# Performance work log

Measured on AMD Instinct MI355X. Metric: run time of the kernel, lower is better.

Reference implementation:

```python
import jax, jax.numpy as jnp
import numpy as np

B, S, D = 2, 2048, 2048
H, KV, HD = 8, 1, 256          # num_heads, num_kv_heads, head_dim
ROPE_BASE = 10000.0
NEG_INF = -1e9


def _rope_cos_sin(position_ids, head_dim, base):
    # position_ids: [B, S] -> cos/sin: [B, S, head_dim]
    inv_freq = 1.0 / (base ** (jnp.arange(0, head_dim, 2, dtype=jnp.float32) / head_dim))
    freqs = position_ids.astype(jnp.float32)[..., None] * inv_freq  # [B,S,HD/2]
    emb = jnp.concatenate([freqs, freqs], axis=-1)                  # [B,S,HD]
    return jnp.cos(emb), jnp.sin(emb)


def _rotate_half(x):
    h = x.shape[-1] // 2
    return jnp.concatenate([-x[..., h:], x[..., :h]], axis=-1)


def _apply_rope(x, cos, sin):
    # x: [B,h,S,HD]; cos/sin: [B,S,HD]
    c = cos[:, None, :, :]
    s = sin[:, None, :, :]
    return x * c + _rotate_half(x) * s


def setup_inputs() -> dict:
    key = jax.random.key(0)
    ks = jax.random.split(key, 6)
    hidden_state = jax.random.normal(ks[0], (B, S, D), dtype=jnp.float32)
    # additive causal mask: 0 on/below diagonal, -inf above
    causal = jnp.tril(jnp.ones((S, S), dtype=bool))
    attention_mask = jnp.where(causal, 0.0, NEG_INF).astype(jnp.float32)[None, None]  # [B?1,1,S,S]
    attention_mask = jnp.broadcast_to(attention_mask, (B, 1, S, S))
    position_ids = jnp.broadcast_to(jnp.arange(S, dtype=jnp.int64)[None, :], (B, S))
    scale = 0.02
    Wq = jax.random.normal(ks[1], (D, H * HD), dtype=jnp.float32) * scale
    Wk = jax.random.normal(ks[2], (D, KV * HD), dtype=jnp.float32) * scale
    Wv = jax.random.normal(ks[3], (D, KV * HD), dtype=jnp.float32) * scale
    Wo = jax.random.normal(ks[4], (H * HD, D), dtype=jnp.float32) * scale
    return {"hidden_state": hidden_state, "attention_mask": attention_mask,
            "position_ids": position_ids, "Wq": Wq, "Wk": Wk, "Wv": Wv, "Wo": Wo}


def reference(hidden_state, attention_mask, position_ids, Wq, Wk, Wv, Wo):
    bsz, q_len, _ = hidden_state.shape
    n_rep = H // KV
    # projections
    q = (hidden_state @ Wq).reshape(bsz, q_len, H, HD).transpose(0, 2, 1, 3)   # [B,H,S,HD]
    k = (hidden_state @ Wk).reshape(bsz, q_len, KV, HD).transpose(0, 2, 1, 3)  # [B,KV,S,HD]
    v = (hidden_state @ Wv).reshape(bsz, q_len, KV, HD).transpose(0, 2, 1, 3)
    # RoPE
    cos, sin = _rope_cos_sin(position_ids, HD, ROPE_BASE)
    q = _apply_rope(q, cos, sin)
    k = _apply_rope(k, cos, sin)
    # GQA: repeat kv heads
    k = jnp.repeat(k, n_rep, axis=1)  # [B,H,S,HD]
    v = jnp.repeat(v, n_rep, axis=1)
    # eager attention with full score matrix (faithful to source)
    scores = jnp.einsum('bhqd,bhkd->bhqk', q, k) / jnp.sqrt(jnp.float32(HD))
    scores = scores + attention_mask
    attn = jax.nn.softmax(scores.astype(jnp.float32), axis=-1).astype(q.dtype)
    out = jnp.einsum('bhqk,bhkd->bhqd', attn, v)            # [B,H,S,HD]
    out = out.transpose(0, 2, 1, 3).reshape(bsz, q_len, H * HD)
    return out @ Wo
```

## Files before the change

kernel.cpp:

```cpp
#include <hip/hip_runtime.h>
#include <cstdint>
#include <cstddef>

#define B_   2
#define S_   2048
#define D_   2048
#define H_   8
#define HD_  256
#define M_   (B_ * S_)
#define NQ_  (H_ * HD_)
#define NKV_ 256

typedef unsigned short u16;
typedef __attribute__((ext_vector_type(8))) short short8v;
typedef __attribute__((ext_vector_type(4))) float f32x4;

__device__ __forceinline__ u16 f2bf_rn(float x) {
    unsigned int u = __float_as_uint(x);
    unsigned int r = u + 0x7FFFu + ((u >> 16) & 1u);
    return (u16)(r >> 16);
}
__device__ __forceinline__ float bf2f(u16 h) {
    return __uint_as_float(((unsigned int)h) << 16);
}

__device__ __forceinline__ void gll16(const u16* g, u16* l) {
    __builtin_amdgcn_global_load_lds(
        (const __attribute__((address_space(1))) void*)(g),
        (__attribute__((address_space(3))) void*)(l), 16, 0, 0);
}

__global__ __launch_bounds__(256) void split_kernel(const float* __restrict__ in,
                                                    u16* __restrict__ hi,
                                                    u16* __restrict__ lo)
{
    const size_t i = ((size_t)blockIdx.x * 256 + threadIdx.x) * 8;
    float4 v0 = *(const float4*)(in + i);
    float4 v1 = *(const float4*)(in + i + 4);
    float xs[8] = {v0.x, v0.y, v0.z, v0.w, v1.x, v1.y, v1.z, v1.w};
    unsigned int hv[4], lv[4];
#pragma unroll
    for (int k = 0; k < 4; ++k) {
        u16 h0 = f2bf_rn(xs[2 * k]);
        u16 h1 = f2bf_rn(xs[2 * k + 1]);
        u16 l0 = f2bf_rn(xs[2 * k] - bf2f(h0));
        u16 l1 = f2bf_rn(xs[2 * k + 1] - bf2f(h1));
        hv[k] = (unsigned int)h0 | ((unsigned int)h1 << 16);
        lv[k] = (unsigned int)l0 | ((unsigned int)l1 << 16);
    }
    *(uint4*)(hi + i) = make_uint4(hv[0], hv[1], hv[2], hv[3]);
    *(uint4*)(lo + i) = make_uint4(lv[0], lv[1], lv[2], lv[3]);
}

__global__ __launch_bounds__(256) void tsplit_kernel(const float* __restrict__ W,
                                                     u16* __restrict__ Th,
                                                     u16* __restrict__ Tl,
                                                     int K, int N)
{
    __shared__ float t[64][65];
    const int kt = blockIdx.x, nt = blockIdx.y;
    const int c4 = (threadIdx.x & 15) * 4;
    const int r  = threadIdx.x >> 4;

#pragma unroll
    for (int s = 0; s < 4; ++s) {
        const int kk = r + s * 16;
        float4 v = *(const float4*)(W + (size_t)(kt * 64 + kk) * N + nt * 64 + c4);
        t[kk][c4 + 0] = v.x;
        t[kk][c4 + 1] = v.y;
        t[kk][c4 + 2] = v.z;
        t[kk][c4 + 3] = v.w;
    }
    __syncthreads();
#pragma unroll
    for (int s = 0; s < 4; ++s) {
        const int nn = r + s * 16;
        unsigned int hv[2], lv[2];
#pragma unroll
        for (int p = 0; p < 2; ++p) {
            u16 h0, h1, l0, l1;
            float x0 = t[c4 + 2 * p][nn];
            float x1 = t[c4 + 2 * p + 1][nn];
            h0 = f2bf_rn(x0); l0 = f2bf_rn(x0 - bf2f(h0));
            h1 = f2bf_rn(x1); l1 = f2bf_rn(x1 - bf2f(h1));
            hv[p] = (unsigned int)h0 | ((unsigned int)h1 << 16);
            lv[p] = (unsigned int)l0 | ((unsigned int)l1 << 16);
        }
        u16* ph = Th + (size_t)(nt * 64 + nn) * K + kt * 64 + c4;
        u16* pl = Tl + (size_t)(nt * 64 + nn) * K + kt * 64 + c4;
        *(uint2*)ph = make_uint2(hv[0], hv[1]);
        *(uint2*)pl = make_uint2(lv[0], lv[1]);
    }
}

__device__ __forceinline__ void mfma_gemm_tile(
    const u16* __restrict__ Ah, const u16* __restrict__ Al,
    const u16* __restrict__ Bh, const u16* __restrict__ Bl,
    float* __restrict__ C, const int Kd, const int ldc,
    const int bm0, const int bn0)
{
    __shared__ u16 ldsAh[128 * 32];
    __shared__ u16 ldsAl[128 * 32];
    __shared__ u16 ldsBh[128 * 32];
    __shared__ u16 ldsBl[128 * 32];

    const int tid  = threadIdx.x;
    const int lane = tid & 63;
    const int w    = tid >> 6;
    const int wr   = w >> 1, wc = w & 1;

    const int srow = w * 32 + (lane >> 2);
    const int schk = (lane & 3) * 8;
    const u16* gAh = Ah + (size_t)(bm0 + srow) * Kd + schk;
    const u16* gAl = Al + (size_t)(bm0 + srow) * Kd + schk;
    const u16* gBh = Bh + (size_t)(bn0 + srow) * Kd + schk;
    const u16* gBl = Bl + (size_t)(bn0 + srow) * Kd + schk;

    f32x4 acc[4][4];
#pragma unroll
    for (int i = 0; i < 4; ++i)
#pragma unroll
        for (int j = 0; j < 4; ++j) acc[i][j] = (f32x4){0.f, 0.f, 0.f, 0.f};

    const int fr = lane & 15;
    const int kb = (lane >> 4) * 8;

    for (int k0 = 0; k0 < Kd; k0 += 32) {
        if (k0) __syncthreads();
#pragma unroll
        for (int c = 0; c < 2; ++c) {
            const size_t go = (size_t)(c * 16) * Kd + k0;
            const int lb = (w * 32 + c * 16) * 32;
            gll16(gAh + go, &ldsAh[lb]);
            gll16(gAl + go, &ldsAl[lb]);
            gll16(gBh + go, &ldsBh[lb]);
            gll16(gBl + go, &ldsBl[lb]);
        }
        __syncthreads();

        short8v a_h[4], a_l[4], b_h[4], b_l[4];
#pragma unroll
        for (int f = 0; f < 4; ++f) {
            const int ra = (wr * 64 + f * 16 + fr) * 32 + kb;
            const int rb = (wc * 64 + f * 16 + fr) * 32 + kb;
            a_h[f] = *(const short8v*)&ldsAh[ra];
            a_l[f] = *(const short8v*)&ldsAl[ra];
            b_h[f] = *(const short8v*)&ldsBh[rb];
            b_l[f] = *(const short8v*)&ldsBl[rb];
        }
#pragma unroll
        for (int i = 0; i < 4; ++i)
#pragma unroll
            for (int j = 0; j < 4; ++j) {
                acc[i][j] = __builtin_amdgcn_mfma_f32_16x16x32_bf16(a_h[i], b_h[j], acc[i][j], 0, 0, 0);
                acc[i][j] = __builtin_amdgcn_mfma_f32_16x16x32_bf16(a_h[i], b_l[j], acc[i][j], 0, 0, 0);
                acc[i][j] = __builtin_amdgcn_mfma_f32_16x16x32_bf16(a_l[i], b_h[j], acc[i][j], 0, 0, 0);
            }
    }

    const int cr = (lane >> 4) * 4;
    const int cc = lane & 15;
#pragma unroll
    for (int i = 0; i < 4; ++i)
#pragma unroll
        for (int j = 0; j < 4; ++j) {
#pragma unroll
            for (int r = 0; r < 4; ++r) {
                C[(size_t)(bm0 + wr * 64 + i * 16 + cr + r) * ldc
                  + (bn0 + wc * 64 + j * 16 + cc)] = acc[i][j][r];
            }
        }
}

__global__ __launch_bounds__(256, 2) void qkv_mfma_kernel(
    const u16* __restrict__ Xh, const u16* __restrict__ Xl,
    const u16* __restrict__ WqTh, const u16* __restrict__ WqTl,
    const u16* __restrict__ WkTh, const u16* __restrict__ WkTl,
    const u16* __restrict__ WvTh, const u16* __restrict__ WvTl,
    float* __restrict__ Qo, float* __restrict__ Ko, float* __restrict__ Vo)
{
    const int bn = blockIdx.x;
    const u16 *Bh, *Bl; float* C; int ldc, col0;
    if (bn < 16)      { Bh = WqTh; Bl = WqTl; C = Qo; ldc = NQ_;  col0 = bn * 128; }
    else if (bn < 18) { Bh = WkTh; Bl = WkTl; C = Ko; ldc = NKV_; col0 = (bn - 16) * 128; }
    else              { Bh = WvTh; Bl = WvTl; C = Vo; ldc = NKV_; col0 = (bn - 18) * 128; }
    mfma_gemm_tile(Xh, Xl, Bh, Bl, C, D_, ldc, blockIdx.y * 128, col0);
}

__global__ __launch_bounds__(256, 2) void out_mfma_kernel(
    const u16* __restrict__ Ch, const u16* __restrict__ Cl,
    const u16* __restrict__ WoTh, const u16* __restrict__ WoTl,
    float* __restrict__ Out)
{
    mfma_gemm_tile(Ch, Cl, WoTh, WoTl, Out, NQ_, D_, blockIdx.y * 128, blockIdx.x * 128);
}

__global__ __launch_bounds__(128) void rope_split_q_kernel(
    const float* __restrict__ Qw, u16* __restrict__ Qh, u16* __restrict__ Ql)
{
    const int row = blockIdx.x;
    const int d = threadIdx.x;
    const int s = row & (S_ - 1);

    const float expo = (float)(2 * d) / (float)HD_;
    const float inv_freq = 1.0f / powf(10000.0f, expo);
    float sn, c;
    sincosf((float)s * inv_freq, &sn, &c);

    const float* qr = Qw + (size_t)row * NQ_;
    u16* qhr = Qh + (size_t)row * NQ_;
    u16* qlr = Ql + (size_t)row * NQ_;
#pragma unroll
    for (int h = 0; h < H_; ++h) {
        float x0 = qr[h * HD_ + d];
        float x1 = qr[h * HD_ + d + 128];
        float y0 = x0 * c - x1 * sn;
        float y1 = x1 * c + x0 * sn;
        u16 h0 = f2bf_rn(y0), h1 = f2bf_rn(y1);
        qhr[h * HD_ + d]       = h0;
        qhr[h * HD_ + d + 128] = h1;
        qlr[h * HD_ + d]       = f2bf_rn(y0 - bf2f(h0));
        qlr[h * HD_ + d + 128] = f2bf_rn(y1 - bf2f(h1));
    }
}

__global__ __launch_bounds__(128) void rope_split_k_swz_kernel(
    const float* __restrict__ Kw, u16* __restrict__ Kh, u16* __restrict__ Kl,
    int* __restrict__ wq)
{
    if (blockIdx.x == 0 && threadIdx.x == 0) *wq = 0;

    const int row = blockIdx.x;
    const int d = threadIdx.x;
    const int s = row & (S_ - 1);
    const int xm = row & 7;

    const float expo = (float)(2 * d) / (float)HD_;
    const float inv_freq = 1.0f / powf(10000.0f, expo);
    float sn, c;
    sincosf((float)s * inv_freq, &sn, &c);

    const float* kr = Kw + (size_t)row * HD_;
    float x0 = kr[d], x1 = kr[d + 128];
    float y0 = x0 * c - x1 * sn;
    float y1 = x1 * c + x0 * sn;
    u16 h0 = f2bf_rn(y0), h1 = f2bf_rn(y1);

    const int o0 = (((d >> 3) ^ xm) << 3) | (d & 7);
    const int o1 = ((((d + 128) >> 3) ^ xm) << 3) | (d & 7);
    Kh[(size_t)row * HD_ + o0] = h0;
    Kh[(size_t)row * HD_ + o1] = h1;
    Kl[(size_t)row * HD_ + o0] = f2bf_rn(y0 - bf2f(h0));
    Kl[(size_t)row * HD_ + o1] = f2bf_rn(y1 - bf2f(h1));
}

#define KVB_ 32
#define PBS_ 44
#define NITEM_ 512

__global__ __launch_bounds__(256, 2) void attn_mfma_kernel(
    const u16* __restrict__ Qh, const u16* __restrict__ Ql,
    const u16* __restrict__ Kh, const u16* __restrict__ Kl,
    const u16* __restrict__ VtH, const u16* __restrict__ VtL,
    u16* __restrict__ Ch, u16* __restrict__ Cl,
    int* __restrict__ wq)
{
    __shared__ u16 kvK[2 * 32 * 256];
    __shared__ u16 kvV[2 * 256 * 32];
    __shared__ u16 pb[2 * 64 * PBS_];
    __shared__ int s_item;

    const int tid = threadIdx.x;
    const int lane = tid & 63;
    const int w = tid >> 6;

    const int fr = lane & 15;
    const int kq = (lane >> 4);
    const int xm = fr & 7;

    const int k_hi = (lane >> 5);
    const int k_ch = lane & 31;
    const int v_dl = w * 64 + (lane >> 2);
    const int v_cc = (lane & 3) * 8;

    while (true) {
        __syncthreads();
        if (tid == 0) s_item = atomicAdd(wq, 1);
        __syncthreads();
        const int item = s_item;
        if (item >= NITEM_) break;

        const int qt = (item < 256) ? (31 - (item >> 4)) : ((item - 256) >> 4);
        const int bh = item & 15;
        const int b = bh >> 3, h = bh & 7;

        short8v qfh[8], qfl[8];
        {
            const size_t qrow = (size_t)(b * S_ + qt * 64 + w * 16 + fr);
            const u16* ph = Qh + qrow * NQ_ + h * HD_ + kq * 8;
            const u16* pl = Ql + qrow * NQ_ + h * HD_ + kq * 8;
#pragma unroll
            for (int ks = 0; ks < 8; ++ks) {
                qfh[ks] = *(const short8v*)(ph + ks * 32);
                qfl[ks] = *(const short8v*)(pl + ks * 32);
            }
        }

        f32x4 oacc[16];
#pragma unroll
        for (int f = 0; f < 16; ++f) oacc[f] = (f32x4){0.f, 0.f, 0.f, 0.f};
        float m_i[4] = {-1e30f, -1e30f, -1e30f, -1e30f};
        float l_i[4] = {0.f, 0.f, 0.f, 0.f};

        const u16* ksrc[2] = {Kh + (size_t)b * S_ * HD_, Kl + (size_t)b * S_ * HD_};
        const u16* vsrc[2] = {VtH + (size_t)b * HD_ * S_, VtL + (size_t)b * HD_ * S_};

        const int nkt = (qt + 1) * 2;

#define STAGE_K(KT)                                                            \
        {                                                                      \
            _Pragma("unroll")                                                  \
            for (int c = 0; c < 2; ++c) {                                      \
                _Pragma("unroll")                                              \
                for (int t = 0; t < 4; ++t) {                                  \
                    const int rl = w * 8 + t * 2 + k_hi;                       \
                    gll16(ksrc[c] + (size_t)((KT) * KVB_ + rl) * HD_ + k_ch * 8, \
                          &kvK[c * 8192 + (w * 2048 + t * 512)]);              \
                }                                                              \
            }                                                                  \
        }

#define STAGE_V(KT)                                                            \
        {                                                                      \
            _Pragma("unroll")                                                  \
            for (int c = 0; c < 2; ++c) {                                      \
                _Pragma("unroll")                                              \
                for (int t = 0; t < 4; ++t) {                                  \
                    gll16(vsrc[c] + (size_t)(v_dl + t * 16) * S_ + (KT) * KVB_ + v_cc, \
                          &kvV[c * 8192 + (w * 2048 + t * 512)]);              \
                }                                                              \
            }                                                                  \
        }

        STAGE_K(0)
        STAGE_V(0)
        __syncthreads();

        for (int kt = 0; kt < nkt; ++kt) {
            const bool more = (kt + 1 < nkt);

            f32x4 s0 = (f32x4){0.f, 0.f, 0.f, 0.f};
            f32x4 s1 = (f32x4){0.f, 0.f, 0.f, 0.f};
#pragma unroll
            for (int ks = 0; ks < 8; ++ks) {
                const int ch = (ks * 4 + kq) ^ xm;
                short8v kh0 = *(const short8v*)&kvK[fr * 256 + ch * 8];
                short8v kh1 = *(const short8v*)&kvK[(16 + fr) * 256 + ch * 8];
                short8v kl0 = *(const short8v*)&kvK[8192 + fr * 256 + ch * 8];
                short8v kl1 = *(const short8v*)&kvK[8192 + (16 + fr) * 256 + ch * 8];
                s0 = __builtin_amdgcn_mfma_f32_16x16x32_bf16(qfh[ks], kh0, s0, 0, 0, 0);
                s1 = __builtin_amdgcn_mfma_f32_16x16x32_bf16(qfh[ks], kh1, s1, 0, 0, 0);
                s0 = __builtin_amdgcn_mfma_f32_16x16x32_bf16(qfh[ks], kl0, s0, 0, 0, 0);
                s1 = __builtin_amdgcn_mfma_f32_16x16x32_bf16(qfh[ks], kl1, s1, 0, 0, 0);
                s0 = __builtin_amdgcn_mfma_f32_16x16x32_bf16(qfl[ks], kh0, s0, 0, 0, 0);
                s1 = __builtin_amdgcn_mfma_f32_16x16x32_bf16(qfl[ks], kh1, s1, 0, 0, 0);
            }

            const int qglob = qt * 64 + w * 16 + kq * 4;
            const int kg = kt * KVB_ + fr;
            float x0v[4], x1v[4], mxl[4];
            bool needl = false;
#pragma unroll
            for (int r = 0; r < 4; ++r) {
                float x0 = s0[r] * 0.0625f;
                float x1 = s1[r] * 0.0625f;
                if (kg > qglob + r)      x0 = -1e30f;
                if (kg + 16 > qglob + r) x1 = -1e30f;
                x0v[r] = x0; x1v[r] = x1;
                mxl[r] = fmaxf(x0, x1);
                needl = needl || (mxl[r] > m_i[r] + 8.0f);
            }
            if (__any((int)needl)) {
#pragma unroll
                for (int r = 0; r < 4; ++r) {
                    float mx = mxl[r];
#pragma unroll
                    for (int off = 1; off < 16; off <<= 1)
                        mx = fmaxf(mx, __shfl_xor(mx, off, 64));
                    const float mnew = fmaxf(m_i[r], mx);
                    const float alpha = __expf(m_i[r] - mnew);
                    l_i[r] *= alpha;
                    m_i[r] = mnew;
#pragma unroll
                    for (int f = 0; f < 16; ++f) oacc[f][r] *= alpha;
                }
            }
#pragma unroll
            for (int r = 0; r < 4; ++r) {
                const float p0 = __expf(x0v[r] - m_i[r]);
                const float p1 = __expf(x1v[r] - m_i[r]);
                float ps = p0 + p1;
#pragma unroll
                for (int off = 1; off < 16; off <<= 1)
                    ps += __shfl_xor(ps, off, 64);
                l_i[r] += ps;

                const int prow = (w * 16 + kq * 4 + r) * PBS_;
                u16 h0 = f2bf_rn(p0), h1 = f2bf_rn(p1);
                pb[prow + fr]                    = h0;
                pb[prow + 16 + fr]               = h1;
                pb[64 * PBS_ + prow + fr]        = f2bf_rn(p0 - bf2f(h0));
                pb[64 * PBS_ + prow + 16 + fr]   = f2bf_rn(p1 - bf2f(h1));
            }
            __syncthreads();

            if (more) STAGE_K(kt + 1)

            {
                short8v pah = *(const short8v*)&pb[(w * 16 + fr) * PBS_ + kq * 8];
                short8v pal = *(const short8v*)&pb[64 * PBS_ + (w * 16 + fr) * PBS_ + kq * 8];
#pragma unroll
                for (int f = 0; f < 16; ++f) {
                    const int vrow = (f * 16 + fr) * 32 + kq * 8;
                    short8v vh = *(const short8v*)&kvV[vrow];
                    short8v vl = *(const short8v*)&kvV[8192 + vrow];
                    oacc[f] = __builtin_amdgcn_mfma_f32_16x16x32_bf16(pah, vh, oacc[f], 0, 0, 0);
                    oacc[f] = __builtin_amdgcn_mfma_f32_16x16x32_bf16(pal, vh, oacc[f], 0, 0, 0);
                    oacc[f] = __builtin_amdgcn_mfma_f32_16x16x32_bf16(pah, vl, oacc[f], 0, 0, 0);
                }
            }
            if (more) {
                __syncthreads();
                STAGE_V(kt + 1)
            }
        }

        {
            const size_t obase = (size_t)(b * S_ + qt * 64 + w * 16 + kq * 4) * NQ_ + h * HD_ + fr;
            u16* ohr = Ch + obase;
            u16* olr = Cl + obase;
#pragma unroll
            for (int r = 0; r < 4; ++r) {
                const float inv_l = 1.0f / l_i[r];
#pragma unroll
                for (int f = 0; f < 16; ++f) {
                    const float v = oacc[f][r] * inv_l;
                    const u16 hh = f2bf_rn(v);
                    ohr[(size_t)r * NQ_ + f * 16] = hh;
                    olr[(size_t)r * NQ_ + f * 16] = f2bf_rn(v - bf2f(hh));
                }
            }
        }
#undef STAGE_K
#undef STAGE_V
    }
}

extern "C" void kernel_launch(void* const* d_in, const int* in_sizes, int n_in,
                              void* d_out, int out_size, void* d_ws, size_t ws_size,
                              hipStream_t stream)
{
    (void)in_sizes; (void)n_in; (void)out_size; (void)ws_size;

    const float* hidden = (const float*)d_in[0];
    const float* Wq = (const float*)d_in[3];
    const float* Wk = (const float*)d_in[4];
    const float* Wv = (const float*)d_in[5];
    const float* Wo = (const float*)d_in[6];
    float* out = (float*)d_out;

    char* ws = (char*)d_ws;
    float* Qw = (float*)(ws + 0);
    u16* Kh2 = (u16*)(ws + 0);
    u16* Kl2 = (u16*)(ws + 2097152u);
    u16* VtH = (u16*)(ws + 4194304u);
    u16* VtL = (u16*)(ws + 6291456u);
    int* wq  = (int*)(ws + 8388608u);
    float* Kw = (float*)(ws + 33554432u);
    float* Vw = (float*)(ws + 37748736u);
    u16* Ch2 = (u16*)(ws + 41943040u);
    u16* Cl2 = (u16*)(ws + 58720256u);
    u16* Ah  = (u16*)(ws + 75497472u);
    u16* Al  = (u16*)(ws + 92274688u);
    u16* WqTh = (u16*)(ws + 109051904u);
    u16* WqTl = (u16*)(ws + 117440512u);
    u16* WkTh = (u16*)(ws + 125829120u);
    u16* WkTl = (u16*)(ws + 126877696u);
    u16* WvTh = (u16*)(ws + 127926272u);
    u16* WvTl = (u16*)(ws + 128974848u);
    u16* WoTh = WqTh;
    u16* WoTl = WqTl;
    u16* Qhb = Ah;
    u16* Qlb = Al;

    split_kernel<<<dim3((M_ * D_) / (256 * 8)), dim3(256), 0, stream>>>(hidden, Ah, Al);

    tsplit_kernel<<<dim3(D_ / 64, NQ_ / 64),  dim3(256), 0, stream>>>(Wq, WqTh, WqTl, D_, NQ_);
    tsplit_kernel<<<dim3(D_ / 64, NKV_ / 64), dim3(256), 0, stream>>>(Wk, WkTh, WkTl, D_, NKV_);
    tsplit_kernel<<<dim3(D_ / 64, NKV_ / 64), dim3(256), 0, stream>>>(Wv, WvTh, WvTl, D_, NKV_);

    qkv_mfma_kernel<<<dim3(20, M_ / 128), dim3(256), 0, stream>>>(
        Ah, Al, WqTh, WqTl, WkTh, WkTl, WvTh, WvTl, Qw, Kw, Vw);

    rope_split_q_kernel<<<dim3(M_), dim3(128), 0, stream>>>(Qw, Qhb, Qlb);
    rope_split_k_swz_kernel<<<dim3(M_), dim3(128), 0, stream>>>(Kw, Kh2, Kl2, wq);

    tsplit_kernel<<<dim3(S_ / 64, NKV_ / 64), dim3(256), 0, stream>>>(
        Vw, VtH, VtL, S_, NKV_);
    tsplit_kernel<<<dim3(S_ / 64, NKV_ / 64), dim3(256), 0, stream>>>(
        Vw + (size_t)S_ * NKV_, VtH + (size_t)HD_ * S_, VtL + (size_t)HD_ * S_, S_, NKV_);

    attn_mfma_kernel<<<dim3(512), dim3(256), 0, stream>>>(
        Qhb, Qlb, Kh2, Kl2, VtH, VtL, Ch2, Cl2, wq);

    tsplit_kernel<<<dim3(NQ_ / 64, D_ / 64), dim3(256), 0, stream>>>(Wo, WoTh, WoTl, NQ_, D_);

    out_mfma_kernel<<<dim3(D_ / 128, M_ / 128), dim3(256), 0, stream>>>(
        Ch2, Cl2, WoTh, WoTl, out);
}
```

Before: 585.5 us.

## Make attention waves independent with direct global K/V loads and static scheduling

The attention kernel no longer stages K and V tiles through shared memory with block-wide barriers and an atomic work queue. Each wave now owns its own 16-row query slice, assigned statically from the block index, and reads K and V fragments straight from global memory, relying on L2/L1 caching. K is stored unswizzled to match. This removes barriers, the atomic queue and LDS staging, but makes each wave re-read K/V from cache rather than sharing tiles across the four waves. It also replaces dynamic load balancing with a fixed long-first ordering. The causal split is finer at 16 rows per wave.

```diff
diff --git a/kernel.cpp b/kernel.cpp
--- a/kernel.cpp
+++ b/kernel.cpp
@@ -224,16 +224,12 @@
     }
 }
 
-__global__ __launch_bounds__(128) void rope_split_k_swz_kernel(
-    const float* __restrict__ Kw, u16* __restrict__ Kh, u16* __restrict__ Kl,
-    int* __restrict__ wq)
-{
-    if (blockIdx.x == 0 && threadIdx.x == 0) *wq = 0;
-
+__global__ __launch_bounds__(128) void rope_split_k_kernel(
+    const float* __restrict__ Kw, u16* __restrict__ Kh, u16* __restrict__ Kl)
+{
     const int row = blockIdx.x;
     const int d = threadIdx.x;
     const int s = row & (S_ - 1);
-    const int xm = row & 7;
 
     const float expo = (float)(2 * d) / (float)HD_;
     const float inv_freq = 1.0f / powf(10000.0f, expo);
@@ -245,30 +241,21 @@
     float y0 = x0 * c - x1 * sn;
     float y1 = x1 * c + x0 * sn;
     u16 h0 = f2bf_rn(y0), h1 = f2bf_rn(y1);
-
-    const int o0 = (((d >> 3) ^ xm) << 3) | (d & 7);
-    const int o1 = ((((d + 128) >> 3) ^ xm) << 3) | (d & 7);
-    Kh[(size_t)row * HD_ + o0] = h0;
-    Kh[(size_t)row * HD_ + o1] = h1;
-    Kl[(size_t)row * HD_ + o0] = f2bf_rn(y0 - bf2f(h0));
-    Kl[(size_t)row * HD_ + o1] = f2bf_rn(y1 - bf2f(h1));
-}
-
-#define KVB_ 32
+    Kh[(size_t)row * HD_ + d]       = h0;
+    Kh[(size_t)row * HD_ + d + 128] = h1;
+    Kl[(size_t)row * HD_ + d]       = f2bf_rn(y0 - bf2f(h0));
+    Kl[(size_t)row * HD_ + d + 128] = f2bf_rn(y1 - bf2f(h1));
+}
+
 #define PBS_ 44
-#define NITEM_ 512
 
 __global__ __launch_bounds__(256, 2) void attn_mfma_kernel(
     const u16* __restrict__ Qh, const u16* __restrict__ Ql,
     const u16* __restrict__ Kh, const u16* __restrict__ Kl,
     const u16* __restrict__ VtH, const u16* __restrict__ VtL,
-    u16* __restrict__ Ch, u16* __restrict__ Cl,
-    int* __restrict__ wq)
-{
-    __shared__ u16 kvK[2 * 32 * 256];
-    __shared__ u16 kvV[2 * 256 * 32];
+    u16* __restrict__ Ch, u16* __restrict__ Cl)
+{
     __shared__ u16 pb[2 * 64 * PBS_];
-    __shared__ int s_item;
 
     const int tid = threadIdx.x;
     const int lane = tid & 63;
@@ -276,183 +263,135 @@
 
     const int fr = lane & 15;
     const int kq = (lane >> 4);
-    const int xm = fr & 7;
-
-    const int k_hi = (lane >> 5);
-    const int k_ch = lane & 31;
-    const int v_dl = w * 64 + (lane >> 2);
-    const int v_cc = (lane & 3) * 8;
-
-    while (true) {
-        __syncthreads();
-        if (tid == 0) s_item = atomicAdd(wq, 1);
-        __syncthreads();
-        const int item = s_item;
-        if (item >= NITEM_) break;
-
-        const int qt = (item < 256) ? (31 - (item >> 4)) : ((item - 256) >> 4);
-        const int bh = item & 15;
-        const int b = bh >> 3, h = bh & 7;
-
-        short8v qfh[8], qfl[8];
+
+    const int g = blockIdx.x * 4 + w;
+    const int j = g >> 4;
+    const int bh = g & 15;
+    const int qg = (j < 64) ? (127 - j) : (j - 64);
+    const int b = bh >> 3, h = bh & 7;
+
+    short8v qfh[8], qfl[8];
+    {
+        const size_t qrow = (size_t)(b * S_ + qg * 16 + fr);
+        const u16* ph = Qh + qrow * NQ_ + h * HD_ + kq * 8;
+        const u16* pl = Ql + qrow * NQ_ + h * HD_ + kq * 8;
+#pragma unroll
+        for (int ks = 0; ks < 8; ++ks) {
+            qfh[ks] = *(const short8v*)(ph + ks * 32);
+            qfl[ks] = *(const short8v*)(pl + ks * 32);
+        }
+    }
+
+    f32x4 oacc[16];
+#pragma unroll
+    for (int f = 0; f < 16; ++f) oacc[f] = (f32x4){0.f, 0.f, 0.f, 0.f};
+    float m_i[4] = {-1e30f, -1e30f, -1e30f, -1e30f};
+    float l_i[4] = {0.f, 0.f, 0.f, 0.f};
+
+    const u16* kbh = Kh + (size_t)(b * S_ + fr) * HD_ + kq * 8;
+    const u16* kbl = Kl + (size_t)(b * S_ + fr) * HD_ + kq * 8;
+    const u16* vbh = VtH + (size_t)(b * HD_ + fr) * S_ + kq * 8;
+    const u16* vbl = VtL + (size_t)(b * HD_ + fr) * S_ + kq * 8;
+
+    const int nkt = (qg >> 1) + 1;
+
+    for (int kt = 0; kt < nkt; ++kt) {
+        f32x4 s0 = (f32x4){0.f, 0.f, 0.f, 0.f};
+        f32x4 s1 = (f32x4){0.f, 0.f, 0.f, 0.f};
+        const u16* kh_p = kbh + (size_t)(kt * 32) * HD_;
+        const u16* kl_p = kbl + (size_t)(kt * 32) * HD_;
+#pragma unroll
+        for (int ks = 0; ks < 8; ++ks) {
+            short8v kh0 = *(const short8v*)(kh_p + ks * 32);
+            short8v kh1 = *(const short8v*)(kh_p + 16 * HD_ + ks * 32);
+            short8v kl0 = *(const short8v*)(kl_p + ks * 32);
+            short8v kl1 = *(const short8v*)(kl_p + 16 * HD_ + ks * 32);
+            s0 = __builtin_amdgcn_mfma_f32_16x16x32_bf16(qfh[ks], kh0, s0, 0, 0, 0);
+            s1 = __builtin_amdgcn_mfma_f32_16x16x32_bf16(qfh[ks], kh1, s1, 0, 0, 0);
+            s0 = __builtin_amdgcn_mfma_f32_16x16x32_bf16(qfh[ks], kl0, s0, 0, 0, 0);
+            s1 = __builtin_amdgcn_mfma_f32_16x16x32_bf16(qfh[ks], kl1, s1, 0, 0, 0);
+            s0 = __builtin_amdgcn_mfma_f32_16x16x32_bf16(qfl[ks], kh0, s0, 0, 0, 0);
+            s1 = __builtin_amdgcn_mfma_f32_16x16x32_bf16(qfl[ks], kh1, s1, 0, 0, 0);
+        }
+
+        const int qglob = qg * 16 + kq * 4;
+        const int kg = kt * 32 + fr;
+        float x0v[4], x1v[4], mxl[4];
+        bool needl = false;
+#pragma unroll
+        for (int r = 0; r < 4; ++r) {
+            float x0 = s0[r] * 0.0625f;
+            float x1 = s1[r] * 0.0625f;
+            if (kg > qglob + r)      x0 = -1e30f;
+            if (kg + 16 > qglob + r) x1 = -1e30f;
+            x0v[r] = x0; x1v[r] = x1;
+            mxl[r] = fmaxf(x0, x1);
+            needl = needl || (mxl[r] > m_i[r] + 8.0f);
+        }
+        if (__any((int)needl)) {
+#pragma unroll
+            for (int r = 0; r < 4; ++r) {
+                float mx = mxl[r];
+#pragma unroll
+                for (int off = 1; off < 16; off <<= 1)
+                    mx = fmaxf(mx, __shfl_xor(mx, off, 64));
+                const float mnew = fmaxf(m_i[r], mx);
+                const float alpha = __expf(m_i[r] - mnew);
+                l_i[r] *= alpha;
+                m_i[r] = mnew;
+#pragma unroll
+                for (int f = 0; f < 16; ++f) oacc[f][r] *= alpha;
+            }
+        }
+#pragma unroll
+        for (int r = 0; r < 4; ++r) {
+            const float p0 = __expf(x0v[r] - m_i[r]);
+            const float p1 = __expf(x1v[r] - m_i[r]);
+            float ps = p0 + p1;
+#pragma unroll
+            for (int off = 1; off < 16; off <<= 1)
+                ps += __shfl_xor(ps, off, 64);
+            l_i[r] += ps;
+
+            const int prow = (w * 16 + kq * 4 + r) * PBS_;
+            u16 h0 = f2bf_rn(p0), h1 = f2bf_rn(p1);
+            pb[prow + fr]                    = h0;
+            pb[prow + 16 + fr]               = h1;
+            pb[64 * PBS_ + prow + fr]        = f2bf_rn(p0 - bf2f(h0));
+            pb[64 * PBS_ + prow + 16 + fr]   = f2bf_rn(p1 - bf2f(h1));
+        }
+
         {
-            const size_t qrow = (size_t)(b * S_ + qt * 64 + w * 16 + fr);
-            const u16* ph = Qh + qrow * NQ_ + h * HD_ + kq * 8;
-            const u16* pl = Ql + qrow * NQ_ + h * HD_ + kq * 8;
-#pragma unroll
-            for (int ks = 0; ks < 8; ++ks) {
-                qfh[ks] = *(const short8v*)(ph + ks * 32);
-                qfl[ks] = *(const short8v*)(pl + ks * 32);
+            short8v pah = *(const short8v*)&pb[(w * 16 + fr) * PBS_ + kq * 8];
+            short8v pal = *(const short8v*)&pb[64 * PBS_ + (w * 16 + fr) * PBS_ + kq * 8];
+            const u16* vh_p = vbh + kt * 32;
+            const u16* vl_p = vbl + kt * 32;
+#pragma unroll
+            for (int f = 0; f < 16; ++f) {
+                short8v vh = *(const short8v*)(vh_p + (size_t)(f * 16) * S_);
+                short8v vl = *(const short8v*)(vl_p + (size_t)(f * 16) * S_);
+                oacc[f] = __builtin_amdgcn_mfma_f32_16x16x32_bf16(pah, vh, oacc[f], 0, 0, 0);
+                oacc[f] = __builtin_amdgcn_mfma_f32_16x16x32_bf16(pal, vh, oacc[f], 0, 0, 0);
+                oacc[f] = __builtin_amdgcn_mfma_f32_16x16x32_bf16(pah, vl, oacc[f], 0, 0, 0);
             }
         }
-
-        f32x4 oacc[16];
-#pragma unroll
-        for (int f = 0; f < 16; ++f) oacc[f] = (f32x4){0.f, 0.f, 0.f, 0.f};
-        float m_i[4] = {-1e30f, -1e30f, -1e30f, -1e30f};
-        float l_i[4] = {0.f, 0.f, 0.f, 0.f};
-
-        const u16* ksrc[2] = {Kh + (size_t)b * S_ * HD_, Kl + (size_t)b * S_ * HD_};
-        const u16* vsrc[2] = {VtH + (size_t)b * HD_ * S_, VtL + (size_t)b * HD_ * S_};
-
-        const int nkt = (qt + 1) * 2;
-
-#define STAGE_K(KT)                                                            \
-        {                                                                      \
-            _Pragma("unroll")                                                  \
-            for (int c = 0; c < 2; ++c) {                                      \
-                _Pragma("unroll")                                              \
-                for (int t = 0; t < 4; ++t) {                                  \
-                    const int rl = w * 8 + t * 2 + k_hi;                       \
-                    gll16(ksrc[c] + (size_t)((KT) * KVB_ + rl) * HD_ + k_ch * 8, \
-                          &kvK[c * 8192 + (w * 2048 + t * 512)]);              \
-                }                                                              \
-            }                                                                  \
-        }
-
-#define STAGE_V(KT)                                                            \
-        {                                                                      \
-            _Pragma("unroll")                                                  \
-            for (int c = 0; c < 2; ++c) {                                      \
-                _Pragma("unroll")                                              \
-                for (int t = 0; t < 4; ++t) {                                  \
-                    gll16(vsrc[c] + (size_t)(v_dl + t * 16) * S_ + (KT) * KVB_ + v_cc, \
-                          &kvV[c * 8192 + (w * 2048 + t * 512)]);              \
-                }                                                              \
-            }                                                                  \
-        }
-
-        STAGE_K(0)
-        STAGE_V(0)
-        __syncthreads();
-
-        for (int kt = 0; kt < nkt; ++kt) {
-            const bool more = (kt + 1 < nkt);
-
-            f32x4 s0 = (f32x4){0.f, 0.f, 0.f, 0.f};
-            f32x4 s1 = (f32x4){0.f, 0.f, 0.f, 0.f};
-#pragma unroll
-            for (int ks = 0; ks < 8; ++ks) {
-                const int ch = (ks * 4 + kq) ^ xm;
-                short8v kh0 = *(const short8v*)&kvK[fr * 256 + ch * 8];
-                short8v kh1 = *(const short8v*)&kvK[(16 + fr) * 256 + ch * 8];
-                short8v kl0 = *(const short8v*)&kvK[8192 + fr * 256 + ch * 8];
-                short8v kl1 = *(const short8v*)&kvK[8192 + (16 + fr) * 256 + ch * 8];
-                s0 = __builtin_amdgcn_mfma_f32_16x16x32_bf16(qfh[ks], kh0, s0, 0, 0, 0);
-                s1 = __builtin_amdgcn_mfma_f32_16x16x32_bf16(qfh[ks], kh1, s1, 0, 0, 0);
-                s0 = __builtin_amdgcn_mfma_f32_16x16x32_bf16(qfh[ks], kl0, s0, 0, 0, 0);
-                s1 = __builtin_amdgcn_mfma_f32_16x16x32_bf16(qfh[ks], kl1, s1, 0, 0, 0);
-                s0 = __builtin_amdgcn_mfma_f32_16x16x32_bf16(qfl[ks], kh0, s0, 0, 0, 0);
-                s1 = __builtin_amdgcn_mfma_f32_16x16x32_bf16(qfl[ks], kh1, s1, 0, 0, 0);
+    }
+
+    {
+        const size_t obase = (size_t)(b * S_ + qg * 16 + kq * 4) * NQ_ + h * HD_ + fr;
+        u16* ohr = Ch + obase;
+        u16* olr = Cl + obase;
+#pragma unroll
+        for (int r = 0; r < 4; ++r) {
+            const float inv_l = 1.0f / l_i[r];
+#pragma unroll
+            for (int f = 0; f < 16; ++f) {
+                const float v = oacc[f][r] * inv_l;
+                const u16 hh = f2bf_rn(v);
+                ohr[(size_t)r * NQ_ + f * 16] = hh;
+                olr[(size_t)r * NQ_ + f * 16] = f2bf_rn(v - bf2f(hh));
             }
-
-            const int qglob = qt * 64 + w * 16 + kq * 4;
-            const int kg = kt * KVB_ + fr;
-            float x0v[4], x1v[4], mxl[4];
-            bool needl = false;
-#pragma unroll
-            for (int r = 0; r < 4; ++r) {
-                float x0 = s0[r] * 0.0625f;
-                float x1 = s1[r] * 0.0625f;
-                if (kg > qglob + r)      x0 = -1e30f;
-                if (kg + 16 > qglob + r) x1 = -1e30f;
-                x0v[r] = x0; x1v[r] = x1;
-                mxl[r] = fmaxf(x0, x1);
-                needl = needl || (mxl[r] > m_i[r] + 8.0f);
-            }
-            if (__any((int)needl)) {
-#pragma unroll
-                for (int r = 0; r < 4; ++r) {
-                    float mx = mxl[r];
-#pragma unroll
-                    for (int off = 1; off < 16; off <<= 1)
-                        mx = fmaxf(mx, __shfl_xor(mx, off, 64));
-                    const float mnew = fmaxf(m_i[r], mx);
-                    const float alpha = __expf(m_i[r] - mnew);
-                    l_i[r] *= alpha;
-                    m_i[r] = mnew;
-#pragma unroll
-                    for (int f = 0; f < 16; ++f) oacc[f][r] *= alpha;
-                }
-            }
-#pragma unroll
-            for (int r = 0; r < 4; ++r) {
-                const float p0 = __expf(x0v[r] - m_i[r]);
-                const float p1 = __expf(x1v[r] - m_i[r]);
-                float ps = p0 + p1;
-#pragma unroll
-                for (int off = 1; off < 16; off <<= 1)
-                    ps += __shfl_xor(ps, off, 64);
-                l_i[r] += ps;
-
-                const int prow = (w * 16 + kq * 4 + r) * PBS_;
-                u16 h0 = f2bf_rn(p0), h1 = f2bf_rn(p1);
-                pb[prow + fr]                    = h0;
-                pb[prow + 16 + fr]               = h1;
-                pb[64 * PBS_ + prow + fr]        = f2bf_rn(p0 - bf2f(h0));
-                pb[64 * PBS_ + prow + 16 + fr]   = f2bf_rn(p1 - bf2f(h1));
-            }
-            __syncthreads();
-
-            if (more) STAGE_K(kt + 1)
-
-            {
-                short8v pah = *(const short8v*)&pb[(w * 16 + fr) * PBS_ + kq * 8];
-                short8v pal = *(const short8v*)&pb[64 * PBS_ + (w * 16 + fr) * PBS_ + kq * 8];
-#pragma unroll
-                for (int f = 0; f < 16; ++f) {
-                    const int vrow = (f * 16 + fr) * 32 + kq * 8;
-                    short8v vh = *(const short8v*)&kvV[vrow];
-                    short8v vl = *(const short8v*)&kvV[8192 + vrow];
-                    oacc[f] = __builtin_amdgcn_mfma_f32_16x16x32_bf16(pah, vh, oacc[f], 0, 0, 0);
-                    oacc[f] = __builtin_amdgcn_mfma_f32_16x16x32_bf16(pal, vh, oacc[f], 0, 0, 0);
-                    oacc[f] = __builtin_amdgcn_mfma_f32_16x16x32_bf16(pah, vl, oacc[f], 0, 0, 0);
-                }
-            }
-            if (more) {
-                __syncthreads();
-                STAGE_V(kt + 1)
-            }
-        }
-
-        {
-            const size_t obase = (size_t)(b * S_ + qt * 64 + w * 16 + kq * 4) * NQ_ + h * HD_ + fr;
-            u16* ohr = Ch + obase;
-            u16* olr = Cl + obase;
-#pragma unroll
-            for (int r = 0; r < 4; ++r) {
-                const float inv_l = 1.0f / l_i[r];
-#pragma unroll
-                for (int f = 0; f < 16; ++f) {
-                    const float v = oacc[f][r] * inv_l;
-                    const u16 hh = f2bf_rn(v);
-                    ohr[(size_t)r * NQ_ + f * 16] = hh;
-                    olr[(size_t)r * NQ_ + f * 16] = f2bf_rn(v - bf2f(hh));
-                }
-            }
-        }
-#undef STAGE_K
-#undef STAGE_V
+        }
     }
 }
 
@@ -475,7 +414,6 @@
     u16* Kl2 = (u16*)(ws + 2097152u);
     u16* VtH = (u16*)(ws + 4194304u);
     u16* VtL = (u16*)(ws + 6291456u);
-    int* wq  = (int*)(ws + 8388608u);
     float* Kw = (float*)(ws + 33554432u);
     float* Vw = (float*)(ws + 37748736u);
     u16* Ch2 = (u16*)(ws + 41943040u);
@@ -503,7 +441,7 @@
         Ah, Al, WqTh, WqTl, WkTh, WkTl, WvTh, WvTl, Qw, Kw, Vw);
 
     rope_split_q_kernel<<<dim3(M_), dim3(128), 0, stream>>>(Qw, Qhb, Qlb);
-    rope_split_k_swz_kernel<<<dim3(M_), dim3(128), 0, stream>>>(Kw, Kh2, Kl2, wq);
+    rope_split_k_kernel<<<dim3(M_), dim3(128), 0, stream>>>(Kw, Kh2, Kl2);
 
     tsplit_kernel<<<dim3(S_ / 64, NKV_ / 64), dim3(256), 0, stream>>>(
         Vw, VtH, VtL, S_, NKV_);
@@ -511,7 +449,7 @@
         Vw + (size_t)S_ * NKV_, VtH + (size_t)HD_ * S_, VtL + (size_t)HD_ * S_, S_, NKV_);
 
     attn_mfma_kernel<<<dim3(512), dim3(256), 0, stream>>>(
-        Qhb, Qlb, Kh2, Kl2, VtH, VtL, Ch2, Cl2, wq);
+        Qhb, Qlb, Kh2, Kl2, VtH, VtL, Ch2, Cl2);
 
     tsplit_kernel<<<dim3(NQ_ / 64, D_ / 64), dim3(256), 0, stream>>>(Wo, WoTh, WoTl, NQ_, D_);
 
```

Measured after the change: 961.1 us. 1.64x slower.
